# Kernel optimization log

Measured on AMD Instinct MI355X. Metric: run time of the kernel, lower is better.

## Reference

```python
import jax, jax.numpy as jnp
import numpy as np

NUM_CHUNKS = 8
TOP_K = 2
IN_F = 4096
HID_F = 4096
OUT_F = 4096
B = 4096


def setup_inputs() -> dict:
    key = jax.random.key(0)
    k = jax.random.split(key, 5)
    cin = IN_F // NUM_CHUNKS    # 512
    cout = HID_F // NUM_CHUNKS  # 512
    s_in = 1.0 / np.sqrt(cin)
    s_fin = 1.0 / np.sqrt(cout * TOP_K)
    return {
        "x": jax.random.normal(k[0], (B, IN_F), dtype=jnp.float32),
        # stacked chunk-expert Linear params: y = x @ W + b
        "W_chunks": jax.random.uniform(k[1], (NUM_CHUNKS, cin, cout), jnp.float32, -s_in, s_in),
        "b_chunks": jax.random.uniform(k[2], (NUM_CHUNKS, cout), jnp.float32, -s_in, s_in),
        "W_final": jax.random.uniform(k[3], (cout * TOP_K, OUT_F), jnp.float32, -s_fin, s_fin),
        "b_final": jax.random.uniform(k[4], (OUT_F,), jnp.float32, -s_fin, s_fin),
    }


def reference(x, W_chunks, b_chunks, W_final, b_final):
    Bsz = x.shape[0]
    # split into chunks along feature dim: (B, num_chunks, chunk_in)
    xr = x.reshape(Bsz, NUM_CHUNKS, -1)
    # per-chunk activity = mean(|chunk|) over the whole batch (matches torch .abs().mean())
    activities = jnp.mean(jnp.abs(xr), axis=(0, 2))  # (num_chunks,)
    _, topk_idx = jax.lax.top_k(activities, TOP_K)    # descending, like torch.topk
    # gather selected chunks and their expert weights, run small GEMMs
    x_sel = xr[:, topk_idx, :]                        # (B, k, chunk_in)
    h = jnp.einsum('bkc,kcd->bkd', x_sel, W_chunks[topk_idx]) + b_chunks[topk_idx]
    h = h.reshape(Bsz, -1)                            # concat along feature dim
    out = h @ W_final + b_final                       # (B, out_features)
    return out
```

## Files before the change

kernel.cpp:

```cpp
#include <hip/hip_runtime.h>


typedef __bf16 bf16x8_t __attribute__((ext_vector_type(8)));
typedef float  f32x4_t  __attribute__((ext_vector_type(4)));
typedef unsigned short u16x4 __attribute__((ext_vector_type(4)));

__device__ inline unsigned short f2bf(float f) {
    __bf16 b = (__bf16)f;
    return __builtin_bit_cast(unsigned short, b);
}

__device__ inline void stage_glds(const unsigned short* gtile, int stride, int row0,
                                  unsigned short* lds, int lane) {
    const int r8 = lane >> 3;
    const int gg = (lane & 7) ^ r8;
    const unsigned short* gp = gtile + (size_t)(row0 + r8) * stride + gg * 8;
    unsigned short* lp = lds + row0 * 64;
    __builtin_amdgcn_global_load_lds((const __attribute__((address_space(1))) void*)gp,
                                     (__attribute__((address_space(3))) void*)lp,
                                     16, 0, 0);
}

__device__ inline bf16x8_t ldsfrag(const unsigned short* Ls, int row, int kb) {
    return *(const bf16x8_t*)(Ls + row * 64 + (((kb >> 3) ^ (row & 7)) * 8));
}

__global__ void fused_prep_kernel(const float* __restrict__ x, const float* __restrict__ Wc,
                                  const float* __restrict__ Wf, float* __restrict__ part,
                                  unsigned short* __restrict__ wct, unsigned short* __restrict__ wft) {
    const int b = blockIdx.x;
    const int tid = threadIdx.x;

    if (b < 512) {
        const int chunk = b & 7;
        const int rg = b >> 3;
        const int colf4 = tid & 127;
        const int rsub = tid >> 7;
        const float4* base = (const float4*)x + (size_t)chunk * 128 + colf4;
        float s = 0.f;
        #pragma unroll 4
        for (int i = 0; i < 32; ++i) {
            int row = rg * 64 + i * 2 + rsub;
            float4 v = base[(size_t)row * 1024];
            s += fabsf(v.x) + fabsf(v.y) + fabsf(v.z) + fabsf(v.w);
        }
        #pragma unroll
        for (int off = 32; off > 0; off >>= 1) s += __shfl_down(s, off, 64);
        __shared__ float wsum[4];
        if ((tid & 63) == 0) wsum[tid >> 6] = s;
        __syncthreads();
        if (tid == 0) part[chunk * 64 + rg] = wsum[0] + wsum[1] + wsum[2] + wsum[3];
        return;
    }

    __shared__ float tile[64][65];
    const float* src; unsigned short* dst; int R, C, cb, rb;
    if (b < 1536) {
        int jj = b - 512;
        src = Wf; dst = wft; R = 1024; C = 4096;
        cb = (jj & 63) * 64; rb = (jj >> 6) * 64;
    } else {
        int jj = b - 1536;
        int c = jj >> 6, t = jj & 63;
        src = Wc + (size_t)c * 262144;
        dst = wct + (size_t)c * 262144;
        R = 512; C = 512;
        cb = (t & 7) * 64; rb = (t >> 3) * 64;
    }
    {
        const int cx = tid & 63;
        const int ry = tid >> 6;
        #pragma unroll
        for (int i = 0; i < 16; ++i)
            tile[ry + i * 4][cx] = src[(size_t)(rb + ry + i * 4) * C + cb + cx];
    }
    __syncthreads();
    {
        const int c16 = tid & 15;
        const int r16 = tid >> 4;
        #pragma unroll
        for (int p = 0; p < 4; ++p) {
            u16x4 hv;
            #pragma unroll
            for (int j = 0; j < 4; ++j) hv[j] = f2bf(tile[c16 * 4 + j][r16 + p * 16]);
            *(u16x4*)(dst + (size_t)(cb + r16 + p * 16) * R + rb + c16 * 4) = hv;
        }
    }
}

__global__ __launch_bounds__(256, 4)
void gemm1_kernel(const float* __restrict__ x, const unsigned short* __restrict__ wct,
                  const float* __restrict__ bc, const float* __restrict__ part,
                  unsigned short* __restrict__ h) {
    __shared__ __align__(16) unsigned char lds_raw[24576];
    unsigned short* As = (unsigned short*)lds_raw;
    unsigned short* Bs = (unsigned short*)(lds_raw + 8192);

    const int tid = threadIdx.x;
    const int wave = tid >> 6;
    const int lane = tid & 63;

    {
        float* sred = (float*)lds_raw;
        sred[tid] = part[tid];
        sred[tid + 256] = part[tid + 256];
        __syncthreads();
        float* act8 = (float*)(lds_raw + 2048);
        if (tid < 8) {
            float a = 0.f;
            #pragma unroll
            for (int k = 0; k < 64; ++k) a += sred[tid * 64 + k];
            act8[tid] = a;
        }
        __syncthreads();
    }
    int sel0, sel1;
    {
        const float* act8 = (const float*)(lds_raw + 2048);
        float v0 = -1e30f, v1 = -1e30f; int b0 = 0, b1 = 0;
        #pragma unroll
        for (int i = 0; i < 8; ++i) {
            float v = act8[i];
            if (v > v0) { v1 = v0; b1 = b0; v0 = v; b0 = i; }
            else if (v > v1) { v1 = v; b1 = i; }
        }
        sel0 = b0; sel1 = b1;
    }
    __syncthreads();

    const int z = blockIdx.z;
    const int idxz = z ? sel1 : sel0;
    const int m0 = blockIdx.x * 64;
    const int n0 = blockIdx.y * 128;
    const int wm = (wave >> 1) * 32;
    const int wn = (wave & 1) * 64;
    const int rl = lane & 15;
    const int quad = lane >> 4;

    const float* xtile = x + (size_t)m0 * 4096 + idxz * 512;
    const unsigned short* Btile = wct + (size_t)idxz * 262144 + (size_t)n0 * 512;

    f32x4_t acc[4][2] = {};
    const int ar = tid >> 2;
    const int aq = tid & 3;

    for (int k0 = 0; k0 < 512; k0 += 64) {
        #pragma unroll
        for (int s = wave; s < 16; s += 4)
            stage_glds(Btile + k0, 512, s * 8, Bs, lane);
        const float* gr = xtile + (size_t)ar * 4096 + k0;
        #pragma unroll
        for (int j = 0; j < 2; ++j) {
            int gg = aq * 2 + j;
            float4 a = *(const float4*)(gr + gg * 8);
            float4 c = *(const float4*)(gr + gg * 8 + 4);
            bf16x8_t v;
            v[0] = (__bf16)a.x; v[1] = (__bf16)a.y; v[2] = (__bf16)a.z; v[3] = (__bf16)a.w;
            v[4] = (__bf16)c.x; v[5] = (__bf16)c.y; v[6] = (__bf16)c.z; v[7] = (__bf16)c.w;
            *(bf16x8_t*)(As + ar * 64 + ((gg ^ (ar & 7)) * 8)) = v;
        }
        __syncthreads();
        #pragma unroll
        for (int kq = 0; kq < 2; ++kq) {
            const int kb = kq * 32 + quad * 8;
            bf16x8_t af[2], bfr[4];
            #pragma unroll
            for (int i = 0; i < 2; ++i) af[i]  = ldsfrag(As, wm + i * 16 + rl, kb);
            #pragma unroll
            for (int i = 0; i < 4; ++i) bfr[i] = ldsfrag(Bs, wn + i * 16 + rl, kb);
            #pragma unroll
            for (int ni = 0; ni < 4; ++ni)
                #pragma unroll
                for (int mi = 0; mi < 2; ++mi)
                    acc[ni][mi] = __builtin_amdgcn_mfma_f32_16x16x32_bf16(bfr[ni], af[mi], acc[ni][mi], 0, 0, 0);
        }
        __syncthreads();
    }

    const float* bias = bc + (size_t)idxz * 512;
    #pragma unroll
    for (int ni = 0; ni < 4; ++ni) {
        const int colb = n0 + wn + ni * 16 + quad * 4;
        f32x4_t bv4 = *(const f32x4_t*)(bias + colb);
        #pragma unroll
        for (int mi = 0; mi < 2; ++mi) {
            int row = m0 + wm + mi * 16 + rl;
            f32x4_t o = acc[ni][mi] + bv4;
            u16x4 hv;
            #pragma unroll
            for (int j = 0; j < 4; ++j) hv[j] = f2bf(o[j]);
            *(u16x4*)(h + (size_t)row * 1024 + z * 512 + colb) = hv;
        }
    }
}

__global__ __launch_bounds__(256, 4)
void gemm2_kernel(const unsigned short* __restrict__ h, const unsigned short* __restrict__ wft,
                  const float* __restrict__ bfin, float* __restrict__ out) {
    __shared__ __align__(16) unsigned short AsBs[2 * 8192];
    unsigned short* As = AsBs;
    unsigned short* Bs = AsBs + 8192;
    const int m0 = blockIdx.x * 128;
    const int n0 = blockIdx.y * 128;
    const int tid = threadIdx.x;
    const int wave = tid >> 6;
    const int lane = tid & 63;
    const int wm = (wave >> 1) * 64;
    const int wn = (wave & 1) * 64;
    const int rl = lane & 15;
    const int quad = lane >> 4;

    const unsigned short* Atile = h + (size_t)m0 * 1024;
    const unsigned short* Btile = wft + (size_t)n0 * 1024;

    f32x4_t acc[4][4] = {};

    for (int k0 = 0; k0 < 1024; k0 += 64) {
        #pragma unroll
        for (int s = wave; s < 32; s += 4) {
            if (s < 16) stage_glds(Atile + k0, 1024, s * 8, As, lane);
            else        stage_glds(Btile + k0, 1024, (s - 16) * 8, Bs, lane);
        }
        __syncthreads();
        #pragma unroll
        for (int kq = 0; kq < 2; ++kq) {
            const int kb = kq * 32 + quad * 8;
            bf16x8_t af[4], bfr[4];
            #pragma unroll
            for (int i = 0; i < 4; ++i) {
                af[i]  = ldsfrag(As, wm + i * 16 + rl, kb);
                bfr[i] = ldsfrag(Bs, wn + i * 16 + rl, kb);
            }
            #pragma unroll
            for (int mi = 0; mi < 4; ++mi)
                #pragma unroll
                for (int ni = 0; ni < 4; ++ni)
                    acc[mi][ni] = __builtin_amdgcn_mfma_f32_16x16x32_bf16(af[mi], bfr[ni], acc[mi][ni], 0, 0, 0);
        }
        __syncthreads();
    }

    float* ebuf = (float*)AsBs;
    float bv[4];
    #pragma unroll
    for (int ni = 0; ni < 4; ++ni) bv[ni] = bfin[n0 + wn + ni * 16 + rl];

    #pragma unroll
    for (int c = 0; c < 2; ++c) {
        if ((wave >> 1) == c) {
            #pragma unroll
            for (int mi = 0; mi < 4; ++mi)
                #pragma unroll
                for (int ni = 0; ni < 4; ++ni)
                    #pragma unroll
                    for (int j = 0; j < 4; ++j)
                        ebuf[(mi * 16 + quad * 4 + j) * 128 + wn + ni * 16 + rl]
                            = acc[mi][ni][j] + bv[ni];
        }
        __syncthreads();
        const int rr8 = tid >> 5;
        const int c4  = tid & 31;
        #pragma unroll
        for (int i = 0; i < 8; ++i) {
            int rr = i * 8 + rr8;
            f32x4_t v = *(const f32x4_t*)(ebuf + rr * 128 + c4 * 4);
            *(f32x4_t*)(out + (size_t)(m0 + c * 64 + rr) * 4096 + n0 + c4 * 4) = v;
        }
        __syncthreads();
    }
}

extern "C" void kernel_launch(void* const* d_in, const int* in_sizes, int n_in,
                              void* d_out, int out_size, void* d_ws, size_t ws_size,
                              hipStream_t stream) {
    const float* x    = (const float*)d_in[0];
    const float* Wc   = (const float*)d_in[1];
    const float* bc   = (const float*)d_in[2];
    const float* Wf   = (const float*)d_in[3];
    const float* bfin = (const float*)d_in[4];
    float* out = (float*)d_out;

    float* part = (float*)d_ws;
    unsigned short* h   = (unsigned short*)((char*)d_ws + 4096);
    unsigned short* wct = h   + (size_t)4096 * 1024;
    unsigned short* wft = wct + (size_t)8 * 512 * 512;

    fused_prep_kernel<<<2048, 256, 0, stream>>>(x, Wc, Wf, part, wct, wft);
    gemm1_kernel<<<dim3(64, 4, 2), 256, 0, stream>>>(x, wct, bc, part, h);
    gemm2_kernel<<<dim3(32, 32, 1), 256, 0, stream>>>(h, wft, bfin, out);
}
```

Measured before the change: 183.1 us.

## Rewrite final GEMM with 256x256 tiles, double-buffered async LDS pipeline

```diff
diff --git a/kernel.cpp b/kernel.cpp
--- a/kernel.cpp
+++ b/kernel.cpp
@@ -23,6 +23,12 @@
 
 __device__ inline bf16x8_t ldsfrag(const unsigned short* Ls, int row, int kb) {
     return *(const bf16x8_t*)(Ls + row * 64 + (((kb >> 3) ^ (row & 7)) * 8));
+}
+
+__device__ inline void stage_half(const unsigned short* ghalf, unsigned short* lhalf,
+                                  int wv, int lane) {
+    stage_glds(ghalf, 1024, wv * 8, lhalf, lane);
+    stage_glds(ghalf, 1024, 64 + wv * 8, lhalf, lane);
 }
 
 __global__ void fused_prep_kernel(const float* __restrict__ x, const float* __restrict__ Wc,
@@ -194,79 +200,104 @@
     }
 }
 
-__global__ __launch_bounds__(256, 4)
+__global__ __launch_bounds__(512, 2)
 void gemm2_kernel(const unsigned short* __restrict__ h, const unsigned short* __restrict__ wft,
                   const float* __restrict__ bfin, float* __restrict__ out) {
-    __shared__ __align__(16) unsigned short AsBs[2 * 8192];
-    unsigned short* As = AsBs;
-    unsigned short* Bs = AsBs + 8192;
-    const int m0 = blockIdx.x * 128;
-    const int n0 = blockIdx.y * 128;
-    const int tid = threadIdx.x;
-    const int wave = tid >> 6;
+    __shared__ __align__(16) unsigned short lds_s[65536];
+
+    const int tid  = threadIdx.x;
+    const int wv   = tid >> 6;
     const int lane = tid & 63;
-    const int wm = (wave >> 1) * 64;
-    const int wn = (wave & 1) * 64;
-    const int rl = lane & 15;
+    const int m0 = blockIdx.x * 256;
+    const int n0 = blockIdx.y * 256;
+    const int wmo = (wv >> 2) * 128;
+    const int wno = (wv & 3) * 64;
+    const int rl   = lane & 15;
     const int quad = lane >> 4;
 
-    const unsigned short* Atile = h + (size_t)m0 * 1024;
+    const unsigned short* Atile = h   + (size_t)m0 * 1024;
     const unsigned short* Btile = wft + (size_t)n0 * 1024;
 
-    f32x4_t acc[4][4] = {};
-
-    for (int k0 = 0; k0 < 1024; k0 += 64) {
-        #pragma unroll
-        for (int s = wave; s < 32; s += 4) {
-            if (s < 16) stage_glds(Atile + k0, 1024, s * 8, As, lane);
-            else        stage_glds(Btile + k0, 1024, (s - 16) * 8, Bs, lane);
-        }
-        __syncthreads();
-        #pragma unroll
-        for (int kq = 0; kq < 2; ++kq) {
-            const int kb = kq * 32 + quad * 8;
-            bf16x8_t af[4], bfr[4];
-            #pragma unroll
-            for (int i = 0; i < 4; ++i) {
-                af[i]  = ldsfrag(As, wm + i * 16 + rl, kb);
-                bfr[i] = ldsfrag(Bs, wn + i * 16 + rl, kb);
-            }
-            #pragma unroll
-            for (int mi = 0; mi < 4; ++mi)
-                #pragma unroll
-                for (int ni = 0; ni < 4; ++ni)
-                    acc[mi][ni] = __builtin_amdgcn_mfma_f32_16x16x32_bf16(af[mi], bfr[ni], acc[mi][ni], 0, 0, 0);
-        }
-        __syncthreads();
-    }
-
-    float* ebuf = (float*)AsBs;
-    float bv[4];
-    #pragma unroll
-    for (int ni = 0; ni < 4; ++ni) bv[ni] = bfin[n0 + wn + ni * 16 + rl];
-
-    #pragma unroll
-    for (int c = 0; c < 2; ++c) {
-        if ((wave >> 1) == c) {
-            #pragma unroll
-            for (int mi = 0; mi < 4; ++mi)
+    f32x4_t acc[8][4] = {};
+
+    stage_half(Btile,                          lds_s + 32768,        wv, lane);
+    stage_half(Btile + (size_t)128 * 1024,     lds_s + 32768 + 8192, wv, lane);
+    stage_half(Atile,                          lds_s,                wv, lane);
+    stage_half(Atile + (size_t)128 * 1024,     lds_s + 8192,         wv, lane);
+    stage_half(Btile + 64,                     lds_s + 49152,        wv, lane);
+    stage_half(Btile + (size_t)128 * 1024 + 64, lds_s + 49152 + 8192, wv, lane);
+    asm volatile("s_waitcnt vmcnt(4)" ::: "memory");
+    __builtin_amdgcn_s_barrier();
+    __builtin_amdgcn_sched_barrier(0);
+
+    #pragma unroll 2
+    for (int t = 0; t < 16; ++t) {
+        const int bd = t & 1;
+        const unsigned short* Acur = lds_s + bd * 16384;
+        const unsigned short* Bcur = lds_s + 32768 + bd * 16384;
+        const int ta = (t + 1 < 16) ? t + 1 : 15;
+        const int tb = (t + 2 < 16) ? t + 2 : 15;
+        unsigned short* Adst = lds_s + ((t + 1) & 1) * 16384;
+        unsigned short* Bdst = lds_s + 32768 + bd * 16384;
+
+        bf16x8_t bf[8];
+        #pragma unroll
+        for (int ph = 0; ph < 4; ++ph) {
+            bf16x8_t af[2][2];
+            if (ph == 0) {
                 #pragma unroll
                 for (int ni = 0; ni < 4; ++ni)
                     #pragma unroll
-                    for (int j = 0; j < 4; ++j)
-                        ebuf[(mi * 16 + quad * 4 + j) * 128 + wn + ni * 16 + rl]
-                            = acc[mi][ni][j] + bv[ni];
-        }
-        __syncthreads();
-        const int rr8 = tid >> 5;
-        const int c4  = tid & 31;
-        #pragma unroll
-        for (int i = 0; i < 8; ++i) {
-            int rr = i * 8 + rr8;
-            f32x4_t v = *(const f32x4_t*)(ebuf + rr * 128 + c4 * 4);
-            *(f32x4_t*)(out + (size_t)(m0 + c * 64 + rr) * 4096 + n0 + c4 * 4) = v;
-        }
-        __syncthreads();
+                    for (int kq = 0; kq < 2; ++kq)
+                        bf[ni * 2 + kq] = ldsfrag(Bcur, wno + ni * 16 + rl, kq * 32 + quad * 8);
+            }
+            #pragma unroll
+            for (int mi = 0; mi < 2; ++mi)
+                #pragma unroll
+                for (int kq = 0; kq < 2; ++kq)
+                    af[mi][kq] = ldsfrag(Acur, wmo + ph * 32 + mi * 16 + rl, kq * 32 + quad * 8);
+
+            if (ph == 0)      stage_half(Atile + ta * 64,                         Adst,        wv, lane);
+            else if (ph == 1) stage_half(Atile + (size_t)128 * 1024 + ta * 64,    Adst + 8192, wv, lane);
+            else if (ph == 2) stage_half(Btile + tb * 64,                         Bdst,        wv, lane);
+            else              stage_half(Btile + (size_t)128 * 1024 + tb * 64,    Bdst + 8192, wv, lane);
+
+            __builtin_amdgcn_sched_barrier(0);
+            __builtin_amdgcn_s_barrier();
+            asm volatile("s_waitcnt lgkmcnt(0)" ::: "memory");
+            __builtin_amdgcn_sched_barrier(0);
+            __builtin_amdgcn_s_setprio(1);
+            #pragma unroll
+            for (int mi = 0; mi < 2; ++mi)
+                #pragma unroll
+                for (int ni = 0; ni < 4; ++ni)
+                    #pragma unroll
+                    for (int kq = 0; kq < 2; ++kq)
+                        acc[ph * 2 + mi][ni] = __builtin_amdgcn_mfma_f32_16x16x32_bf16(
+                            af[mi][kq], bf[ni * 2 + kq], acc[ph * 2 + mi][ni], 0, 0, 0);
+            __builtin_amdgcn_s_setprio(0);
+            __builtin_amdgcn_sched_barrier(0);
+            if (ph == 3) asm volatile("s_waitcnt vmcnt(4)" ::: "memory");
+            __builtin_amdgcn_s_barrier();
+            __builtin_amdgcn_sched_barrier(0);
+        }
+    }
+    asm volatile("s_waitcnt vmcnt(0)" ::: "memory");
+
+    const int row_l = quad * 4;
+    float bv[4];
+    #pragma unroll
+    for (int ni = 0; ni < 4; ++ni) bv[ni] = bfin[n0 + wno + ni * 16 + rl];
+    #pragma unroll
+    for (int j = 0; j < 4; ++j) {
+        #pragma unroll
+        for (int MI = 0; MI < 8; ++MI) {
+            int row = m0 + wmo + MI * 16 + row_l + j;
+            float* orow = out + (size_t)row * 4096 + n0 + wno + rl;
+            #pragma unroll
+            for (int ni = 0; ni < 4; ++ni)
+                orow[ni * 16] = acc[MI][ni][j] + bv[ni];
+        }
     }
 }
 
@@ -287,5 +318,5 @@
 
     fused_prep_kernel<<<2048, 256, 0, stream>>>(x, Wc, Wf, part, wct, wft);
     gemm1_kernel<<<dim3(64, 4, 2), 256, 0, stream>>>(x, wct, bc, part, h);
-    gemm2_kernel<<<dim3(32, 32, 1), 256, 0, stream>>>(h, wft, bfin, out);
-}
+    gemm2_kernel<<<dim3(16, 16, 1), 512, 0, stream>>>(h, wft, bfin, out);
+}
```

Result: no change. 182.5 us (-0.3%).
